# Optimization experiments

Hardware: AMD Instinct MI355X
Metric: run time of the kernel (lower is better)

The kernel has to match this reference:

```python
import jax, jax.numpy as jnp
import numpy as np

DIM, HEADS, DIM_HEAD = 1024, 16, 64
INNER = HEADS * DIM_HEAD  # 1024
FF = 4 * DIM
EPS = 1e-5


def layer_norm(x, g, b):
    mu = jnp.mean(x, axis=-1, keepdims=True)
    var = jnp.mean(jnp.square(x - mu), axis=-1, keepdims=True)
    return (x - mu) * jax.lax.rsqrt(var + EPS) * g + b


def setup_inputs() -> dict:
    key = jax.random.key(0)
    ks = jax.random.split(key, 8)
    B, N = 2, 2048
    s = 0.02
    return {
        "x": jax.random.normal(ks[0], (B, N, DIM), dtype=jnp.float32),
        "ln1_g": jnp.ones((DIM,), jnp.float32),
        "ln1_b": jnp.zeros((DIM,), jnp.float32),
        "ln2_g": jnp.ones((DIM,), jnp.float32),
        "ln2_b": jnp.zeros((DIM,), jnp.float32),
        "w_qkv": jax.random.normal(ks[1], (DIM, 3 * INNER), jnp.float32) * s,
        "w_out": jax.random.normal(ks[2], (INNER, DIM), jnp.float32) * s,
        "b_out": jnp.zeros((DIM,), jnp.float32),
        "w_ff1": jax.random.normal(ks[3], (DIM, FF), jnp.float32) * s,
        "b_ff1": jnp.zeros((FF,), jnp.float32),
        "w_ff2": jax.random.normal(ks[4], (FF, DIM), jnp.float32) * s,
        "b_ff2": jnp.zeros((DIM,), jnp.float32),
    }


def reference(x, ln1_g, ln1_b, ln2_g, ln2_b, w_qkv, w_out, b_out,
              w_ff1, b_ff1, w_ff2, b_ff2):
    B, N, _ = x.shape
    scale = DIM_HEAD ** -0.5
    h = layer_norm(x, ln1_g, ln1_b)
    qkv = h @ w_qkv  # [B, N, 3*INNER]
    q, k, v = jnp.split(qkv, 3, axis=-1)
    # b n (h d) -> b h n d
    def to_heads(t):
        return t.reshape(B, N, HEADS, DIM_HEAD).transpose(0, 2, 1, 3)
    q, k, v = to_heads(q), to_heads(k), to_heads(v)
    dots = jnp.einsum('bhnd,bhmd->bhnm', q, k) * scale
    attn = jax.nn.softmax(dots, axis=-1)  # dropout = identity (eval)
    out = jnp.einsum('bhnm,bhmd->bhnd', attn, v)
    out = out.transpose(0, 2, 1, 3).reshape(B, N, INNER)
    out = out @ w_out + b_out
    x = x + out  # residual
    h2 = layer_norm(x, ln2_g, ln2_b)
    ff = jax.nn.gelu(h2 @ w_ff1 + b_ff1, approximate=False) @ w_ff2 + b_ff2
    return x + ff
```

## Files before the change

kernel.cpp:

```cpp
#include <hip/hip_runtime.h>
#include <hip/hip_bf16.h>
#include <math.h>

#define SEQ   2048
#define BATCH 2
#define NROWS 4096
#define DIMM  1024
#define QKV3  3072
#define FFD   4096
#define NHEAD 16
#define DHEAD 64

typedef __bf16 bf16;
typedef __bf16 bf16x4 __attribute__((ext_vector_type(4)));
typedef __bf16 bf16x8 __attribute__((ext_vector_type(8)));
typedef float  f32x4  __attribute__((ext_vector_type(4)));

static __device__ __forceinline__ f32x4 mfma16(bf16x8 a, bf16x8 b, f32x4 c) {
    return __builtin_amdgcn_mfma_f32_16x16x32_bf16(a, b, c, 0, 0, 0);
}

#define GLDS16(gp, lp) __builtin_amdgcn_global_load_lds( \
    (__attribute__((address_space(1))) void*)(gp),       \
    (__attribute__((address_space(3))) void*)(lp), 16, 0, 0)

__global__ __launch_bounds__(256) void tcast_kernel(
    const float* __restrict__ src, bf16* __restrict__ dst, int K, int N)
{
    __shared__ float tile[32][33];
    const int n0 = blockIdx.x * 32;
    const int k0 = blockIdx.y * 32;
    const int r = threadIdx.x >> 5;
    const int c = threadIdx.x & 31;
    #pragma unroll
    for (int i = 0; i < 4; ++i)
        tile[r + 8 * i][c] = src[(size_t)(k0 + r + 8 * i) * N + n0 + c];
    __syncthreads();
    #pragma unroll
    for (int i = 0; i < 4; ++i)
        dst[(size_t)(n0 + r + 8 * i) * K + k0 + c] = (bf16)tile[c][r + 8 * i];
}

__global__ __launch_bounds__(256) void ln_cast_kernel(
    const float* __restrict__ x, const float* __restrict__ g,
    const float* __restrict__ b, bf16* __restrict__ out)
{
    const int row = blockIdx.x;
    const int t = threadIdx.x;
    const float4 v = ((const float4*)(x + (size_t)row * DIMM))[t];
    float s  = v.x + v.y + v.z + v.w;
    float sq = v.x * v.x + v.y * v.y + v.z * v.z + v.w * v.w;
    #pragma unroll
    for (int m = 1; m < 64; m <<= 1) {
        s  += __shfl_xor(s, m, 64);
        sq += __shfl_xor(sq, m, 64);
    }
    __shared__ float ss[4], ssq[4];
    const int wave = t >> 6;
    if ((t & 63) == 0) { ss[wave] = s; ssq[wave] = sq; }
    __syncthreads();
    s  = ss[0] + ss[1] + ss[2] + ss[3];
    sq = ssq[0] + ssq[1] + ssq[2] + ssq[3];
    const float mean = s * (1.0f / DIMM);
    const float var  = sq * (1.0f / DIMM) - mean * mean;
    const float rs   = rsqrtf(var + 1e-5f);
    const float4 gv = ((const float4*)g)[t];
    const float4 bv = ((const float4*)b)[t];
    bf16* o = out + (size_t)row * DIMM + t * 4;
    o[0] = (bf16)((v.x - mean) * rs * gv.x + bv.x);
    o[1] = (bf16)((v.y - mean) * rs * gv.y + bv.y);
    o[2] = (bf16)((v.z - mean) * rs * gv.z + bv.z);
    o[3] = (bf16)((v.w - mean) * rs * gv.w + bv.w);
}

template<int EPI>
__global__ __launch_bounds__(256, 3)
void gemm_bt_kernel(const bf16* __restrict__ A, const bf16* __restrict__ BT,
                    const float* __restrict__ bias, const float* __restrict__ res,
                    void* __restrict__ Cout, int M, int N, int K, int ld)
{
    __shared__ bf16 As[3][4096];
    __shared__ bf16 Bs[3][4096];
    const int nb = N >> 7;
    const int chunk = (int)gridDim.x >> 3;
    int idx = (blockIdx.x & 7) * chunk + (blockIdx.x >> 3);
    int ks = 0;
    if (EPI == 3) {
        const int tiles = (M >> 7) * nb;
        ks = idx / tiles;
        idx -= ks * tiles;
    }
    const int bm = idx / nb, bn = idx - bm * nb;
    const int tm = bm << 7, tn = bn << 7;
    const int tid = threadIdx.x;
    const int lane = tid & 63, wave = tid >> 6;
    const int wm = (wave >> 1) << 6, wn = (wave & 1) << 6;
    const int kofs = ks * K;

    const bf16* ga = A  + (size_t)(tm + wave * 32 + (lane >> 2)) * ld + kofs + ((lane & 3) << 3);
    const bf16* gb = BT + (size_t)(tn + wave * 32 + (lane >> 2)) * ld + kofs + ((lane & 3) << 3);
    const size_t k16 = (size_t)16 * ld;

    f32x4 acc[4][4] = {};
    const int ro = (lane & 15) * 32 + ((lane >> 4) << 3);

#define GSTAGE(BUF, KO) do {                          \
        bf16* la_ = &As[BUF][wave * 1024];            \
        bf16* lb_ = &Bs[BUF][wave * 1024];            \
        GLDS16(ga + (KO),       la_);                 \
        GLDS16(ga + (KO) + k16, la_ + 512);           \
        GLDS16(gb + (KO),       lb_);                 \
        GLDS16(gb + (KO) + k16, lb_ + 512);           \
    } while (0)

    GSTAGE(0, 0);
    GSTAGE(1, 32);
    GSTAGE(2, 64);
    int cur = 0;
    for (int k0 = 0; k0 < K; k0 += 32) {
        if (k0 + 96 <= K)      asm volatile("s_waitcnt vmcnt(8)" ::: "memory");
        else if (k0 + 64 <= K) asm volatile("s_waitcnt vmcnt(4)" ::: "memory");
        else                   asm volatile("s_waitcnt vmcnt(0)" ::: "memory");
        __builtin_amdgcn_s_barrier();

        bf16x8 af[4], bfr[4];
        #pragma unroll
        for (int i = 0; i < 4; ++i) {
            af[i]  = *(const bf16x8*)(&As[cur][0] + (wm + i * 16) * 32 + ro);
            bfr[i] = *(const bf16x8*)(&Bs[cur][0] + (wn + i * 16) * 32 + ro);
        }
        #pragma unroll
        for (int i = 0; i < 4; ++i)
            #pragma unroll
            for (int j = 0; j < 4; ++j)
                acc[i][j] = mfma16(af[i], bfr[j], acc[i][j]);

        asm volatile("" ::: "memory");
        __builtin_amdgcn_s_barrier();
        asm volatile("" ::: "memory");
        if (k0 + 96 < K) GSTAGE(cur, k0 + 96);
        cur = (cur == 2) ? 0 : cur + 1;
    }
#undef GSTAGE

    const int r0 = tm + wm + ((lane >> 4) << 2);
    const int c0 = tn + wn + (lane & 15);
    if (EPI == 0) {
        bf16* C = (bf16*)Cout;
        #pragma unroll
        for (int i = 0; i < 4; ++i)
            #pragma unroll
            for (int j = 0; j < 4; ++j)
                #pragma unroll
                for (int r = 0; r < 4; ++r)
                    C[(size_t)(r0 + i * 16 + r) * N + (c0 + j * 16)] = (bf16)acc[i][j][r];
    } else if (EPI == 1) {
        float* C = (float*)Cout;
        #pragma unroll
        for (int j = 0; j < 4; ++j) {
            const float bv = bias[c0 + j * 16];
            #pragma unroll
            for (int i = 0; i < 4; ++i)
                #pragma unroll
                for (int r = 0; r < 4; ++r) {
                    const size_t idx2 = (size_t)(r0 + i * 16 + r) * N + (c0 + j * 16);
                    C[idx2] = acc[i][j][r] + bv + res[idx2];
                }
        }
    } else if (EPI == 2) {
        bf16* C = (bf16*)Cout;
        #pragma unroll
        for (int j = 0; j < 4; ++j) {
            const float bv = bias[c0 + j * 16];
            #pragma unroll
            for (int i = 0; i < 4; ++i)
                #pragma unroll
                for (int r = 0; r < 4; ++r) {
                    const float v = acc[i][j][r] + bv;
                    const float gl = 0.5f * v * (1.0f + erff(v * 0.70710678118654752f));
                    C[(size_t)(r0 + i * 16 + r) * N + (c0 + j * 16)] = (bf16)gl;
                }
        }
    } else {
        float* C = (float*)(ks == 0 ? Cout : (void*)res);
        #pragma unroll
        for (int j = 0; j < 4; ++j)
            #pragma unroll
            for (int i = 0; i < 4; ++i)
                #pragma unroll
                for (int r = 0; r < 4; ++r)
                    C[(size_t)(r0 + i * 16 + r) * N + (c0 + j * 16)] = acc[i][j][r];
    }
}

__global__ __launch_bounds__(256) void ff2_reduce_kernel(
    const float* __restrict__ p0, const float* __restrict__ p1,
    const float* __restrict__ bias, const float* __restrict__ res,
    float* __restrict__ out)
{
    const int i = blockIdx.x * 256 + threadIdx.x;
    const float4 a = ((const float4*)p0)[i];
    const float4 b = ((const float4*)p1)[i];
    const float4 r = ((const float4*)res)[i];
    const float4 g = ((const float4*)bias)[i & 255];
    float4 o;
    o.x = a.x + b.x + r.x + g.x;
    o.y = a.y + b.y + r.y + g.y;
    o.z = a.z + b.z + r.z + g.z;
    o.w = a.w + b.w + r.w + g.w;
    ((float4*)out)[i] = o;
}

__global__ __launch_bounds__(256) void vtrans_kernel(
    const bf16* __restrict__ qkv, bf16* __restrict__ vT)
{
    __shared__ bf16 t[64 * 64];
    const int n0 = blockIdx.x * 64;
    const int bh = blockIdx.y;
    const int b = bh >> 4, h = bh & 15;
    const bf16* src = qkv + (size_t)(b * SEQ + n0) * QKV3 + 2 * DIMM + h * DHEAD;

    #pragma unroll
    for (int it = 0; it < 2; ++it) {
        const int c = it * 256 + threadIdx.x;
        const int n = c >> 3, d8 = (c & 7) * 8;
        const bf16x8 v8 = *(const bf16x8*)(src + (size_t)n * QKV3 + d8);
        const int byte = (n * 128 + d8 * 2) ^ (((n >> 3) & 7) << 4);
        *(bf16x8*)((char*)t + byte) = v8;
    }
    __syncthreads();
    #pragma unroll
    for (int it = 0; it < 2; ++it) {
        const int c = it * 256 + threadIdx.x;
        const int d = c >> 3, nc = c & 7;
        bf16x8 o8;
        #pragma unroll
        for (int i = 0; i < 8; ++i) {
            const int n = nc * 8 + i;
            const int byte = (n * 128 + d * 2) ^ ((nc & 7) << 4);
            o8[i] = *(const bf16*)((const char*)t + byte);
        }
        *(bf16x8*)(vT + (size_t)bh * DHEAD * SEQ + (size_t)d * SEQ + n0 + nc * 8) = o8;
    }
}

__global__ __launch_bounds__(256, 4)
void attn_kernel(const bf16* __restrict__ qkv, const bf16* __restrict__ vT,
                 bf16* __restrict__ out)
{
    __shared__ bf16 Ks[2][64 * 64];
    __shared__ bf16 Vs[2][64 * 64];
    __shared__ bf16 Ps[4][16 * 64];
    const int bid = blockIdx.x;
    const int idx = (bid & 7) * 128 + (bid >> 3);
    const int qt = idx & 31;
    const int bh = idx >> 5;
    const int b = bh >> 4, h = bh & 15;
    const int tid = threadIdx.x;
    const int lane = tid & 63, wave = tid >> 6;
    const int q = lane & 15, hi = lane >> 4;

    const bf16* qbase = qkv + (size_t)(b * SEQ) * QKV3 + h * DHEAD;
    const bf16* kbase = qbase + DIMM;
    const bf16* vbase = vT + (size_t)bh * DHEAD * SEQ;

    const int q0 = qt * 64 + wave * 16;
    bf16x8 qf[2];
    {
        const bf16* qp = qbase + (size_t)(q0 + q) * QKV3 + (hi << 3);
        qf[0] = *(const bf16x8*)qp;
        qf[1] = *(const bf16x8*)(qp + 32);
        #pragma unroll
        for (int j = 0; j < 8; ++j) {
            qf[0][j] = (bf16)((float)qf[0][j] * 0.125f);
            qf[1][j] = (bf16)((float)qf[1][j] * 0.125f);
        }
    }

    const int srow = lane >> 3;
    const int scol = ((lane & 7) ^ srow) << 3;
    const bf16* gk = kbase + (size_t)(wave * 16 + srow) * QKV3 + scol;
    const bf16* gv = vbase + (size_t)(wave * 16 + srow) * SEQ + scol;

#define STAGE(BUF, KT) do {                                        \
        bf16* lk_ = &Ks[BUF][wave * 1024];                         \
        bf16* lv_ = &Vs[BUF][wave * 1024];                         \
        GLDS16(gk + (size_t)(KT) * QKV3,       lk_);               \
        GLDS16(gk + (size_t)((KT) + 8) * QKV3, lk_ + 512);         \
        GLDS16(gv + (KT),                      lv_);               \
        GLDS16(gv + (KT) + 8 * SEQ,            lv_ + 512);         \
    } while (0)

    float m = -1e30f, l = 0.0f;
    f32x4 o[4] = {};

    STAGE(0, 0);
    int cur = 0;
    for (int kt = 0; kt < SEQ; kt += 64) {
        __syncthreads();
        if (kt + 64 < SEQ) STAGE(cur ^ 1, kt + 64);

        f32x4 sv[4];
        __builtin_amdgcn_s_setprio(1);
        #pragma unroll
        for (int kf = 0; kf < 4; ++kf) {
            f32x4 z = {0.f, 0.f, 0.f, 0.f};
            sv[kf] = z;
            #pragma unroll
            for (int ks = 0; ks < 2; ++ks) {
                const int row = kf * 16 + q;
                const int bo = (row * 128 + ks * 64 + (hi << 4)) ^ ((row & 7) << 4);
                const bf16x8 kfrag = *(const bf16x8*)((const char*)&Ks[cur][0] + bo);
                sv[kf] = mfma16(kfrag, qf[ks], sv[kf]);
            }
        }
        __builtin_amdgcn_s_setprio(0);

        float pmax;
        {
            float a = fmaxf(fmaxf(sv[0][0], sv[0][1]), fmaxf(sv[0][2], sv[0][3]));
            float b2 = fmaxf(fmaxf(sv[1][0], sv[1][1]), fmaxf(sv[1][2], sv[1][3]));
            float c = fmaxf(fmaxf(sv[2][0], sv[2][1]), fmaxf(sv[2][2], sv[2][3]));
            float d = fmaxf(fmaxf(sv[3][0], sv[3][1]), fmaxf(sv[3][2], sv[3][3]));
            pmax = fmaxf(fmaxf(a, b2), fmaxf(c, d));
        }
        pmax = fmaxf(pmax, __shfl_xor(pmax, 16, 64));
        pmax = fmaxf(pmax, __shfl_xor(pmax, 32, 64));

        if (__any(pmax - m > 8.0f)) {
            const float nm = fmaxf(m, pmax);
            const float fr = __expf(m - nm);
            l *= fr;
            #pragma unroll
            for (int df = 0; df < 4; ++df) {
                o[df][0] *= fr; o[df][1] *= fr;
                o[df][2] *= fr; o[df][3] *= fr;
            }
            m = nm;
        }

        float rsum = 0.0f;
        #pragma unroll
        for (int kf = 0; kf < 4; ++kf) {
            float p0 = __expf(sv[kf][0] - m);
            float p1 = __expf(sv[kf][1] - m);
            float p2 = __expf(sv[kf][2] - m);
            float p3 = __expf(sv[kf][3] - m);
            rsum += (p0 + p1) + (p2 + p3);
            bf16x4 pk = { (bf16)p0, (bf16)p1, (bf16)p2, (bf16)p3 };
            const int bo = (q * 128 + kf * 32 + hi * 8) ^ ((q & 7) << 4);
            *(bf16x4*)((char*)Ps[wave] + bo) = pk;
        }
        rsum += __shfl_xor(rsum, 16, 64);
        rsum += __shfl_xor(rsum, 32, 64);
        l += rsum;

        bf16x8 pf[2];
        #pragma unroll
        for (int ks = 0; ks < 2; ++ks) {
            const int bo = (q * 128 + ks * 64 + (hi << 4)) ^ ((q & 7) << 4);
            pf[ks] = *(const bf16x8*)((const char*)Ps[wave] + bo);
        }
        __builtin_amdgcn_s_setprio(1);
        #pragma unroll
        for (int df = 0; df < 4; ++df)
            #pragma unroll
            for (int ks = 0; ks < 2; ++ks) {
                const int rowv = df * 16 + q;
                const int bo = (rowv * 128 + ks * 64 + (hi << 4)) ^ ((rowv & 7) << 4);
                const bf16x8 vfrag = *(const bf16x8*)((const char*)&Vs[cur][0] + bo);
                o[df] = mfma16(vfrag, pf[ks], o[df]);
            }
        __builtin_amdgcn_s_setprio(0);
        cur ^= 1;
    }
#undef STAGE

    {
        const float inv = 1.0f / l;
        const int grow = b * SEQ + q0 + q;
        #pragma unroll
        for (int df = 0; df < 4; ++df) {
            bf16x4 pk = { (bf16)(o[df][0] * inv), (bf16)(o[df][1] * inv),
                          (bf16)(o[df][2] * inv), (bf16)(o[df][3] * inv) };
            *(bf16x4*)(out + (size_t)grow * DIMM + h * DHEAD + df * 16 + hi * 4) = pk;
        }
    }
}

extern "C" void kernel_launch(void* const* d_in, const int* in_sizes, int n_in,
                              void* d_out, int out_size, void* d_ws, size_t ws_size,
                              hipStream_t stream)
{
    (void)in_sizes; (void)n_in; (void)out_size;
    const float* x    = (const float*)d_in[0];
    const float* ln1g = (const float*)d_in[1];
    const float* ln1b = (const float*)d_in[2];
    const float* ln2g = (const float*)d_in[3];
    const float* ln2b = (const float*)d_in[4];
    const float* wqkv = (const float*)d_in[5];
    const float* wout = (const float*)d_in[6];
    const float* bout = (const float*)d_in[7];
    const float* wff1 = (const float*)d_in[8];
    const float* bff1 = (const float*)d_in[9];
    const float* wff2 = (const float*)d_in[10];
    const float* bff2 = (const float*)d_in[11];

    char* ws = (char*)d_ws;
    const dim3 blk(256);
    const bool splitk = ws_size >= 92274688ULL;

    if (splitk) {
        bf16*  wff2T = (bf16*)(ws);
        bf16*  woutT = (bf16*)(ws + 8388608);
        bf16*  wff1T = (bf16*)(ws + 10485760);
        bf16*  wqkvT = (bf16*)(ws + 18874368);
        bf16*  hbuf  = (bf16*)(ws + 25165824);
        bf16*  qkvb  = (bf16*)(ws + 33554432);
        bf16*  vT    = (bf16*)(ws + 58720256);
        bf16*  attnb = (bf16*)(ws + 67108864);
        float* x2    = (float*)(ws + 75497472);
        bf16*  fbuf  = (bf16*)(ws + 41943040);
        float* p0    = (float*)(ws + 8388608);
        float* p1    = (float*)(ws + 25165824);

        tcast_kernel<<<dim3(QKV3 / 32, DIMM / 32), blk, 0, stream>>>(wqkv, wqkvT, DIMM, QKV3);
        tcast_kernel<<<dim3(DIMM / 32, DIMM / 32), blk, 0, stream>>>(wout, woutT, DIMM, DIMM);
        tcast_kernel<<<dim3(FFD  / 32, DIMM / 32), blk, 0, stream>>>(wff1, wff1T, DIMM, FFD);
        tcast_kernel<<<dim3(DIMM / 32, FFD  / 32), blk, 0, stream>>>(wff2, wff2T, FFD, DIMM);

        ln_cast_kernel<<<NROWS, blk, 0, stream>>>(x, ln1g, ln1b, hbuf);
        gemm_bt_kernel<0><<<(NROWS / 128) * (QKV3 / 128), blk, 0, stream>>>(
            hbuf, wqkvT, nullptr, nullptr, qkvb, NROWS, QKV3, DIMM, DIMM);
        vtrans_kernel<<<dim3(SEQ / 64, BATCH * NHEAD), blk, 0, stream>>>(qkvb, vT);
        attn_kernel<<<dim3(1024), blk, 0, stream>>>(qkvb, vT, attnb);
        gemm_bt_kernel<1><<<(NROWS / 128) * (DIMM / 128), blk, 0, stream>>>(
            attnb, woutT, bout, x, x2, NROWS, DIMM, DIMM, DIMM);
        ln_cast_kernel<<<NROWS, blk, 0, stream>>>(x2, ln2g, ln2b, hbuf);
        gemm_bt_kernel<2><<<(NROWS / 128) * (FFD / 128), blk, 0, stream>>>(
            hbuf, wff1T, bff1, nullptr, fbuf, NROWS, FFD, DIMM, DIMM);
        gemm_bt_kernel<3><<<2 * (NROWS / 128) * (DIMM / 128), blk, 0, stream>>>(
            fbuf, wff2T, nullptr, (const float*)p1, p0, NROWS, DIMM, FFD / 2, FFD);
        ff2_reduce_kernel<<<(NROWS * DIMM) / 1024, blk, 0, stream>>>(
            p0, p1, bff2, x2, (float*)d_out);
    } else {
        bf16*  wqkvT = (bf16*)(ws);
        bf16*  woutT = (bf16*)(ws + 6291456);
        bf16*  wff1T = (bf16*)(ws + 8388608);
        bf16*  wff2T = (bf16*)(ws + 16777216);
        float* x2    = (float*)(ws + 25165824);
        bf16*  vT    = (bf16*)(ws + 25165824);
        bf16*  hbuf  = (bf16*)(ws + 41943040);
        bf16*  qkvb  = (bf16*)(ws + 50331648);
        bf16*  attnb = (bf16*)(ws + 75497472);
        bf16*  fbuf  = (bf16*)(ws + 50331648);

        tcast_kernel<<<dim3(QKV3 / 32, DIMM / 32), blk, 0, stream>>>(wqkv, wqkvT, DIMM, QKV3);
        tcast_kernel<<<dim3(DIMM / 32, DIMM / 32), blk, 0, stream>>>(wout, woutT, DIMM, DIMM);
        tcast_kernel<<<dim3(FFD  / 32, DIMM / 32), blk, 0, stream>>>(wff1, wff1T, DIMM, FFD);
        tcast_kernel<<<dim3(DIMM / 32, FFD  / 32), blk, 0, stream>>>(wff2, wff2T, FFD, DIMM);

        ln_cast_kernel<<<NROWS, blk, 0, stream>>>(x, ln1g, ln1b, hbuf);
        gemm_bt_kernel<0><<<(NROWS / 128) * (QKV3 / 128), blk, 0, stream>>>(
            hbuf, wqkvT, nullptr, nullptr, qkvb, NROWS, QKV3, DIMM, DIMM);
        vtrans_kernel<<<dim3(SEQ / 64, BATCH * NHEAD), blk, 0, stream>>>(qkvb, vT);
        attn_kernel<<<dim3(1024), blk, 0, stream>>>(qkvb, vT, attnb);
        gemm_bt_kernel<1><<<(NROWS / 128) * (DIMM / 128), blk, 0, stream>>>(
            attnb, woutT, bout, x, x2, NROWS, DIMM, DIMM, DIMM);
        ln_cast_kernel<<<NROWS, blk, 0, stream>>>(x2, ln2g, ln2b, hbuf);
        gemm_bt_kernel<2><<<(NROWS / 128) * (FFD / 128), blk, 0, stream>>>(
            hbuf, wff1T, bff1, nullptr, fbuf, NROWS, FFD, DIMM, DIMM);
        gemm_bt_kernel<1><<<(NROWS / 128) * (DIMM / 128), blk, 0, stream>>>(
            fbuf, wff2T, bff2, x2, (float*)d_out, NROWS, DIMM, FFD, FFD);
    }
}
```

Measured before the change: 277.6 us.

## Add 256x256-tile 512-thread GEMM kernel for QKV and FF1 projections

```diff
diff --git a/kernel.cpp b/kernel.cpp
--- a/kernel.cpp
+++ b/kernel.cpp
@@ -74,6 +74,123 @@
 }
 
 template<int EPI>
+__global__ __launch_bounds__(512, 2)
+void gemm256_kernel(const bf16* __restrict__ A, const bf16* __restrict__ BT,
+                    const float* __restrict__ bias, bf16* __restrict__ C,
+                    int M, int N, int K, int ld)
+{
+    __shared__ bf16 As_[2][2][8192];
+    __shared__ bf16 Bs_[2][2][8192];
+    const int nb = N >> 8;
+    const int chunk = (int)gridDim.x >> 3;
+    const int idx = ((int)blockIdx.x & 7) * chunk + ((int)blockIdx.x >> 3);
+    const int bm = idx / nb, bn = idx - bm * nb;
+    const int tm = bm << 8, tn = bn << 8;
+    const int tid = threadIdx.x;
+    const int lane = tid & 63, w = tid >> 6;
+    const int wr = w >> 2, wc = w & 3;
+    const int lq = lane & 15, hk = lane >> 4;
+
+    const int sr  = lane >> 3;
+    const int sgo = (((lane & 7) ^ sr) << 3);
+    const bf16* gA0 = A  + (size_t)(tm +       w * 8 + sr) * ld + sgo;
+    const bf16* gA1 = A  + (size_t)(tm + 128 + w * 8 + sr) * ld + sgo;
+    const bf16* gB0 = BT + (size_t)(tn +       w * 8 + sr) * ld + sgo;
+    const bf16* gB1 = BT + (size_t)(tn + 128 + w * 8 + sr) * ld + sgo;
+    const size_t l64 = (size_t)64 * ld;
+
+#define STG(D, T) do {                                                   \
+        const size_t ko_ = (size_t)(T) * 64;                             \
+        GLDS16(gA0 + ko_,       &As_[D][0][w * 512]);                    \
+        GLDS16(gA0 + ko_ + l64, &As_[D][0][4096 + w * 512]);             \
+        GLDS16(gA1 + ko_,       &As_[D][1][w * 512]);                    \
+        GLDS16(gA1 + ko_ + l64, &As_[D][1][4096 + w * 512]);             \
+        GLDS16(gB0 + ko_,       &Bs_[D][0][w * 512]);                    \
+        GLDS16(gB0 + ko_ + l64, &Bs_[D][0][4096 + w * 512]);             \
+        GLDS16(gB1 + ko_,       &Bs_[D][1][w * 512]);                    \
+        GLDS16(gB1 + ko_ + l64, &Bs_[D][1][4096 + w * 512]);             \
+    } while (0)
+
+    f32x4 acc[8][4] = {};
+
+    const int NT = K >> 6;
+    STG(0, 0);
+    STG(1, 1);
+    for (int t = 0; t < NT; ++t) {
+        const int d = t & 1;
+        if (t + 1 < NT) asm volatile("s_waitcnt vmcnt(8)" ::: "memory");
+        else            asm volatile("s_waitcnt vmcnt(0)" ::: "memory");
+        __builtin_amdgcn_s_barrier();
+
+        const char* Ah = (const char*)&As_[d][wr][0];
+        const char* Bh = (const char*)&Bs_[d][wc >> 1][0];
+        #pragma unroll
+        for (int q = 0; q < 4; ++q) {
+            const int mb = (q >> 1) * 4, nb2 = (q & 1) * 2;
+            bf16x8 af[4][2], bfv[2][2];
+            #pragma unroll
+            for (int mi = 0; mi < 4; ++mi) {
+                const int lr = (mb + mi) * 16 + lq;
+                #pragma unroll
+                for (int kk = 0; kk < 2; ++kk) {
+                    const int g = kk * 4 + hk;
+                    af[mi][kk] = *(const bf16x8*)(Ah + lr * 128 + ((g ^ (lr & 7)) << 4));
+                }
+            }
+            #pragma unroll
+            for (int nj = 0; nj < 2; ++nj) {
+                const int lc = (wc & 1) * 64 + (nb2 + nj) * 16 + lq;
+                #pragma unroll
+                for (int kk = 0; kk < 2; ++kk) {
+                    const int g = kk * 4 + hk;
+                    bfv[nj][kk] = *(const bf16x8*)(Bh + lc * 128 + ((g ^ (lc & 7)) << 4));
+                }
+            }
+            __builtin_amdgcn_s_setprio(1);
+            #pragma unroll
+            for (int mi = 0; mi < 4; ++mi)
+                #pragma unroll
+                for (int nj = 0; nj < 2; ++nj)
+                    #pragma unroll
+                    for (int kk = 0; kk < 2; ++kk)
+                        acc[mb + mi][nb2 + nj] =
+                            mfma16(af[mi][kk], bfv[nj][kk], acc[mb + mi][nb2 + nj]);
+            __builtin_amdgcn_s_setprio(0);
+        }
+
+        asm volatile("" ::: "memory");
+        __builtin_amdgcn_s_barrier();
+        if (t + 2 < NT) STG(d, t + 2);
+    }
+#undef STG
+
+    const int r0 = tm + wr * 128 + hk * 4;
+    const int c0 = tn + wc * 64 + lq;
+    if (EPI == 0) {
+        #pragma unroll
+        for (int i = 0; i < 8; ++i)
+            #pragma unroll
+            for (int j = 0; j < 4; ++j)
+                #pragma unroll
+                for (int r = 0; r < 4; ++r)
+                    C[(size_t)(r0 + i * 16 + r) * N + (c0 + j * 16)] = (bf16)acc[i][j][r];
+    } else {
+        #pragma unroll
+        for (int j = 0; j < 4; ++j) {
+            const float bv = bias[c0 + j * 16];
+            #pragma unroll
+            for (int i = 0; i < 8; ++i)
+                #pragma unroll
+                for (int r = 0; r < 4; ++r) {
+                    const float v = acc[i][j][r] + bv;
+                    const float gl = 0.5f * v * (1.0f + erff(v * 0.70710678118654752f));
+                    C[(size_t)(r0 + i * 16 + r) * N + (c0 + j * 16)] = (bf16)gl;
+                }
+        }
+    }
+}
+
+template<int EPI>
 __global__ __launch_bounds__(256, 3)
 void gemm_bt_kernel(const bf16* __restrict__ A, const bf16* __restrict__ BT,
                     const float* __restrict__ bias, const float* __restrict__ res,
@@ -145,16 +262,7 @@
 
     const int r0 = tm + wm + ((lane >> 4) << 2);
     const int c0 = tn + wn + (lane & 15);
-    if (EPI == 0) {
-        bf16* C = (bf16*)Cout;
-        #pragma unroll
-        for (int i = 0; i < 4; ++i)
-            #pragma unroll
-            for (int j = 0; j < 4; ++j)
-                #pragma unroll
-                for (int r = 0; r < 4; ++r)
-                    C[(size_t)(r0 + i * 16 + r) * N + (c0 + j * 16)] = (bf16)acc[i][j][r];
-    } else if (EPI == 1) {
+    if (EPI == 1) {
         float* C = (float*)Cout;
         #pragma unroll
         for (int j = 0; j < 4; ++j) {
@@ -165,20 +273,6 @@
                 for (int r = 0; r < 4; ++r) {
                     const size_t idx2 = (size_t)(r0 + i * 16 + r) * N + (c0 + j * 16);
                     C[idx2] = acc[i][j][r] + bv + res[idx2];
-                }
-        }
-    } else if (EPI == 2) {
-        bf16* C = (bf16*)Cout;
-        #pragma unroll
-        for (int j = 0; j < 4; ++j) {
-            const float bv = bias[c0 + j * 16];
-            #pragma unroll
-            for (int i = 0; i < 4; ++i)
-                #pragma unroll
-                for (int r = 0; r < 4; ++r) {
-                    const float v = acc[i][j][r] + bv;
-                    const float gl = 0.5f * v * (1.0f + erff(v * 0.70710678118654752f));
-                    C[(size_t)(r0 + i * 16 + r) * N + (c0 + j * 16)] = (bf16)gl;
                 }
         }
     } else {
@@ -408,6 +502,7 @@
 
     char* ws = (char*)d_ws;
     const dim3 blk(256);
+    const dim3 blk512(512);
     const bool splitk = ws_size >= 92274688ULL;
 
     if (splitk) {
@@ -430,15 +525,15 @@
         tcast_kernel<<<dim3(DIMM / 32, FFD  / 32), blk, 0, stream>>>(wff2, wff2T, FFD, DIMM);
 
         ln_cast_kernel<<<NROWS, blk, 0, stream>>>(x, ln1g, ln1b, hbuf);
-        gemm_bt_kernel<0><<<(NROWS / 128) * (QKV3 / 128), blk, 0, stream>>>(
-            hbuf, wqkvT, nullptr, nullptr, qkvb, NROWS, QKV3, DIMM, DIMM);
+        gemm256_kernel<0><<<(NROWS / 256) * (QKV3 / 256), blk512, 0, stream>>>(
+            hbuf, wqkvT, nullptr, qkvb, NROWS, QKV3, DIMM, DIMM);
         vtrans_kernel<<<dim3(SEQ / 64, BATCH * NHEAD), blk, 0, stream>>>(qkvb, vT);
         attn_kernel<<<dim3(1024), blk, 0, stream>>>(qkvb, vT, attnb);
         gemm_bt_kernel<1><<<(NROWS / 128) * (DIMM / 128), blk, 0, stream>>>(
             attnb, woutT, bout, x, x2, NROWS, DIMM, DIMM, DIMM);
         ln_cast_kernel<<<NROWS, blk, 0, stream>>>(x2, ln2g, ln2b, hbuf);
-        gemm_bt_kernel<2><<<(NROWS / 128) * (FFD / 128), blk, 0, stream>>>(
-            hbuf, wff1T, bff1, nullptr, fbuf, NROWS, FFD, DIMM, DIMM);
+        gemm256_kernel<2><<<(NROWS / 256) * (FFD / 256), blk512, 0, stream>>>(
+            hbuf, wff1T, bff1, fbuf, NROWS, FFD, DIMM, DIMM);
         gemm_bt_kernel<3><<<2 * (NROWS / 128) * (DIMM / 128), blk, 0, stream>>>(
             fbuf, wff2T, nullptr, (const float*)p1, p0, NROWS, DIMM, FFD / 2, FFD);
         ff2_reduce_kernel<<<(NROWS * DIMM) / 1024, blk, 0, stream>>>(
@@ -461,15 +556,15 @@
         tcast_kernel<<<dim3(DIMM / 32, FFD  / 32), blk, 0, stream>>>(wff2, wff2T, FFD, DIMM);
 
         ln_cast_kernel<<<NROWS, blk, 0, stream>>>(x, ln1g, ln1b, hbuf);
-        gemm_bt_kernel<0><<<(NROWS / 128) * (QKV3 / 128), blk, 0, stream>>>(
-            hbuf, wqkvT, nullptr, nullptr, qkvb, NROWS, QKV3, DIMM, DIMM);
+        gemm256_kernel<0><<<(NROWS / 256) * (QKV3 / 256), blk512, 0, stream>>>(
+            hbuf, wqkvT, nullptr, qkvb, NROWS, QKV3, DIMM, DIMM);
         vtrans_kernel<<<dim3(SEQ / 64, BATCH * NHEAD), blk, 0, stream>>>(qkvb, vT);
         attn_kernel<<<dim3(1024), blk, 0, stream>>>(qkvb, vT, attnb);
         gemm_bt_kernel<1><<<(NROWS / 128) * (DIMM / 128), blk, 0, stream>>>(
             attnb, woutT, bout, x, x2, NROWS, DIMM, DIMM, DIMM);
         ln_cast_kernel<<<NROWS, blk, 0, stream>>>(x2, ln2g, ln2b, hbuf);
-        gemm_bt_kernel<2><<<(NROWS / 128) * (FFD / 128), blk, 0, stream>>>(
-            hbuf, wff1T, bff1, nullptr, fbuf, NROWS, FFD, DIMM, DIMM);
+        gemm256_kernel<2><<<(NROWS / 256) * (FFD / 256), blk512, 0, stream>>>(
+            hbuf, wff1T, bff1, fbuf, NROWS, FFD, DIMM, DIMM);
         gemm_bt_kernel<1><<<(NROWS / 128) * (DIMM / 128), blk, 0, stream>>>(
             fbuf, wff2T, bff2, x2, (float*)d_out, NROWS, DIMM, FFD, FFD);
     }
```

Measured after the change: 270.9 us. 2.4% less time.
